# Performance work log

Hardware: AMD Instinct MI355X
Metric: run time of the kernel (lower is better)

Reference implementation:

```python
import jax, jax.numpy as jnp
import numpy as np

# Model constants (from init_kwargs)
N_EMBD = 1024
N_HEAD = 16
HEAD_DIM = N_EMBD // N_HEAD  # 64
SEQ = 32       # new tokens (ds.input_ids)
PAST = 32768   # cached tokens (ds.past)
NEG = -10000.0 # module uses -1e4, not -inf


def setup_inputs() -> dict:
    key = jax.random.key(0)
    ks = jax.random.split(key, 5)
    return {
        "x": jax.random.normal(ks[0], (SEQ, N_EMBD), jnp.float32),
        "layer_past": jax.random.normal(ks[1], (2, N_HEAD, PAST, HEAD_DIM), jnp.float32) * 0.02,
        "w_attn": jax.random.normal(ks[2], (N_EMBD, 3 * N_EMBD), jnp.float32) * 0.02,
        "b_attn": jnp.zeros((3 * N_EMBD,), jnp.float32),
        "w_proj": jax.random.normal(ks[3], (N_EMBD, N_EMBD), jnp.float32) * 0.02,
        "b_proj": jnp.zeros((N_EMBD,), jnp.float32),
        "seq_len": SEQ,
        "past_len": PAST,
    }


def reference(x, layer_past, w_attn, b_attn, w_proj, b_proj, seq_len, past_len):
    # c_attn (Conv1D): x @ W + b, W is [nx, nf]
    qkv = x @ w_attn + b_attn                      # [S, 3E]
    qkv = qkv.reshape(seq_len, 3, N_EMBD)
    # split_heads: [S, E] -> [S, H, D] -> [H, S, D]
    def split(t):
        return t.reshape(seq_len, N_HEAD, HEAD_DIM).transpose(1, 0, 2)
    q, k, v = split(qkv[:, 0]), split(qkv[:, 1]), split(qkv[:, 2])
    # KV-cache concat along time
    key_full = jnp.concatenate([layer_past[0], k], axis=1)   # [H, P+S, D]
    val_full = jnp.concatenate([layer_past[1], v], axis=1)   # [H, P+S, D]
    present = jnp.stack([key_full, val_full])                # [2, H, P+S, D]
    tot_len = past_len + seq_len
    # scores
    w = jnp.einsum("hsd,htd->hst", q, key_full) / float(np.sqrt(HEAD_DIM))
    # causal mask: query at abs position past+i sees keys 0..past+i
    mask = jnp.arange(tot_len)[None, :] <= (past_len + jnp.arange(seq_len))[:, None]
    w = jnp.where(mask[None, :, :], w, NEG)
    w = jax.nn.softmax(w, axis=-1)
    a = jnp.einsum("hst,htd->hsd", w, val_full)              # [H, S, D]
    # merge_heads: [H, S, D] -> [S, H, D] -> [S, E]
    a = a.transpose(1, 0, 2).reshape(seq_len, N_EMBD)
    out = a @ w_proj + b_proj                                # [S, E]
    return (out, present)
```

## Files before the change

### kernel.cpp

```cpp
#include <hip/hip_runtime.h>

#define HEADS 16
#define SEQL 32
#define HD 64
#define PASTN 32768
#define TOTN 32800
#define NE 1024
#define CHUNK 1024
#define NPC 32
#define NCHUNK 33
#define KT 64
#define LDP 68
#define NEGV -10000.0f

__global__ __launch_bounds__(256) void qkv_kernel(
    const float* __restrict__ x, const float* __restrict__ w,
    const float* __restrict__ b, float* __restrict__ qws,
    float* __restrict__ present)
{
    int idx = blockIdx.x * 256 + threadIdx.x;
    int s = idx / 3072;
    int col = idx - s * 3072;
    const float4* x4 = (const float4*)(x + s * NE);
    float a0 = 0.f, a1 = 0.f, a2 = 0.f, a3 = 0.f;
#pragma unroll 8
    for (int k4 = 0; k4 < NE / 4; ++k4) {
        float4 xv = x4[k4];
        const float* wp = w + (k4 * 4) * 3072 + col;
        a0 = fmaf(xv.x, wp[0],        a0);
        a1 = fmaf(xv.y, wp[3072],     a1);
        a2 = fmaf(xv.z, wp[2 * 3072], a2);
        a3 = fmaf(xv.w, wp[3 * 3072], a3);
    }
    float acc = b[col] + ((a0 + a1) + (a2 + a3));
    int g = col >> 10;
    int e = col & 1023;
    int h = e >> 6, d = e & 63;
    if (g == 0)
        qws[(h * SEQL + s) * HD + d] = acc;
    else
        present[(((g - 1) * HEADS + h) * TOTN + PASTN + s) * HD + d] = acc;
}

__global__ __launch_bounds__(256) void attn_partial(
    const float* __restrict__ past, const float* __restrict__ qws,
    float* __restrict__ present, float* __restrict__ opart,
    float* __restrict__ mws, float* __restrict__ lws)
{
    int h = blockIdx.x / NCHUNK;
    int c = blockIdx.x - h * NCHUNK;
    __shared__ __align__(16) float Qs[SEQL][LDP];
    __shared__ __align__(16) float Ks[KT][LDP];
    __shared__ __align__(16) float Vs[KT][LDP];
    __shared__ __align__(16) float Ss[SEQL][LDP];
    __shared__ float mrow[SEQL], lrow[SEQL], arow[SEQL];
    int tid = threadIdx.x;

    for (int i = tid; i < SEQL * 16; i += 256) {
        int q = i >> 4, s4 = i & 15;
        *(float4*)&Qs[q][s4 * 4] = *(const float4*)&qws[(h * SEQL + q) * HD + s4 * 4];
    }
    if (tid < SEQL) { mrow[tid] = -3e38f; lrow[tid] = 0.f; }

    float4 acc4[4];
#pragma unroll
    for (int j = 0; j < 4; ++j) acc4[j] = make_float4(0.f, 0.f, 0.f, 0.f);

    int qg = tid >> 4;
    int lg = tid & 15;
    int nkeys = (c < NPC) ? CHUNK : KT;
    int kstart = c * CHUNK;
    __syncthreads();

    for (int t0 = 0; t0 < nkeys; t0 += KT) {
        if (c < NPC) {
#pragma unroll
            for (int rep = 0; rep < 4; ++rep) {
                int i = tid + rep * 256;
                int row = i >> 4, s4 = i & 15;
                int grow = kstart + t0 + row;
                float4 kk = *(const float4*)&past[(h * PASTN + grow) * HD + s4 * 4];
                float4 vv = *(const float4*)&past[((HEADS + h) * PASTN + grow) * HD + s4 * 4];
                *(float4*)&present[(h * TOTN + grow) * HD + s4 * 4] = kk;
                *(float4*)&present[((HEADS + h) * TOTN + grow) * HD + s4 * 4] = vv;
                *(float4*)&Ks[row][s4 * 4] = kk;
                *(float4*)&Vs[row][s4 * 4] = vv;
            }
        } else {
            float* vz = &Vs[SEQL][0];
            for (int i = tid; i < (KT - SEQL) * LDP; i += 256) vz[i] = 0.f;
#pragma unroll
            for (int rep = 0; rep < 2; ++rep) {
                int i = tid + rep * 256;
                int row = i >> 4, s4 = i & 15;
                int grow = PASTN + row;
                float4 kk = *(const float4*)&present[(h * TOTN + grow) * HD + s4 * 4];
                float4 vv = *(const float4*)&present[((HEADS + h) * TOTN + grow) * HD + s4 * 4];
                *(float4*)&Ks[row][s4 * 4] = kk;
                *(float4*)&Vs[row][s4 * 4] = vv;
            }
        }
        __syncthreads();

        if (tid < 128) {
            float s[4][4];
#pragma unroll
            for (int j = 0; j < 4; ++j)
#pragma unroll
                for (int u = 0; u < 4; ++u) s[j][u] = 0.f;
#pragma unroll
            for (int d4 = 0; d4 < 16; ++d4) {
                float4 qv[4], kv[4];
#pragma unroll
                for (int j = 0; j < 4; ++j)
                    qv[j] = *(const float4*)&Qs[qg * 4 + j][d4 * 4];
#pragma unroll
                for (int u = 0; u < 4; ++u)
                    kv[u] = *(const float4*)&Ks[lg + u * 16][d4 * 4];
#pragma unroll
                for (int j = 0; j < 4; ++j)
#pragma unroll
                    for (int u = 0; u < 4; ++u) {
                        s[j][u] = fmaf(qv[j].x, kv[u].x, s[j][u]);
                        s[j][u] = fmaf(qv[j].y, kv[u].y, s[j][u]);
                        s[j][u] = fmaf(qv[j].z, kv[u].z, s[j][u]);
                        s[j][u] = fmaf(qv[j].w, kv[u].w, s[j][u]);
                    }
            }
#pragma unroll
            for (int j = 0; j < 4; ++j) {
                int q = qg * 4 + j;
#pragma unroll
                for (int u = 0; u < 4; ++u) {
                    float sv = s[j][u] * 0.125f;
                    if (c == NPC && (lg + u * 16) > q) sv = NEGV;
                    Ss[q][lg + u * 16] = sv;
                }
            }
        }
        __syncthreads();

        {
            int q = tid >> 3, sub = tid & 7;
            float v[8];
#pragma unroll
            for (int i = 0; i < 8; ++i) v[i] = Ss[q][sub + 8 * i];
            float mt = fmaxf(fmaxf(fmaxf(v[0], v[1]), fmaxf(v[2], v[3])),
                             fmaxf(fmaxf(v[4], v[5]), fmaxf(v[6], v[7])));
            mt = fmaxf(mt, __shfl_xor(mt, 1));
            mt = fmaxf(mt, __shfl_xor(mt, 2));
            mt = fmaxf(mt, __shfl_xor(mt, 4));
            float mold = mrow[q];
            float mnew = fmaxf(mold, mt);
            float ls = 0.f;
#pragma unroll
            for (int i = 0; i < 8; ++i) {
                float p = __expf(v[i] - mnew);
                Ss[q][sub + 8 * i] = p;
                ls += p;
            }
            ls += __shfl_xor(ls, 1);
            ls += __shfl_xor(ls, 2);
            ls += __shfl_xor(ls, 4);
            if (sub == 0) {
                float alpha = __expf(mold - mnew);
                lrow[q] = lrow[q] * alpha + ls;
                mrow[q] = mnew;
                arow[q] = alpha;
            }
        }
        __syncthreads();

        if (tid < 128) {
#pragma unroll
            for (int j = 0; j < 4; ++j) {
                float aj = arow[qg * 4 + j];
                acc4[j].x *= aj; acc4[j].y *= aj; acc4[j].z *= aj; acc4[j].w *= aj;
            }
#pragma unroll
            for (int t4 = 0; t4 < 16; ++t4) {
                float4 vv[4];
#pragma unroll
                for (int u = 0; u < 4; ++u)
                    vv[u] = *(const float4*)&Vs[t4 * 4 + u][lg * 4];
#pragma unroll
                for (int j = 0; j < 4; ++j) {
                    float4 p = *(const float4*)&Ss[qg * 4 + j][t4 * 4];
                    acc4[j].x = fmaf(p.x, vv[0].x, acc4[j].x);
                    acc4[j].x = fmaf(p.y, vv[1].x, acc4[j].x);
                    acc4[j].x = fmaf(p.z, vv[2].x, acc4[j].x);
                    acc4[j].x = fmaf(p.w, vv[3].x, acc4[j].x);
                    acc4[j].y = fmaf(p.x, vv[0].y, acc4[j].y);
                    acc4[j].y = fmaf(p.y, vv[1].y, acc4[j].y);
                    acc4[j].y = fmaf(p.z, vv[2].y, acc4[j].y);
                    acc4[j].y = fmaf(p.w, vv[3].y, acc4[j].y);
                    acc4[j].z = fmaf(p.x, vv[0].z, acc4[j].z);
                    acc4[j].z = fmaf(p.y, vv[1].z, acc4[j].z);
                    acc4[j].z = fmaf(p.z, vv[2].z, acc4[j].z);
                    acc4[j].z = fmaf(p.w, vv[3].z, acc4[j].z);
                    acc4[j].w = fmaf(p.x, vv[0].w, acc4[j].w);
                    acc4[j].w = fmaf(p.y, vv[1].w, acc4[j].w);
                    acc4[j].w = fmaf(p.z, vv[2].w, acc4[j].w);
                    acc4[j].w = fmaf(p.w, vv[3].w, acc4[j].w);
                }
            }
        }
        __syncthreads();
    }

    if (tid < SEQL) {
        mws[(h * NCHUNK + c) * SEQL + tid] = mrow[tid];
        lws[(h * NCHUNK + c) * SEQL + tid] = lrow[tid];
    }
    if (tid < 128) {
#pragma unroll
        for (int j = 0; j < 4; ++j) {
            int q = qg * 4 + j;
            *(float4*)&opart[((h * NCHUNK + c) * SEQL + q) * HD + lg * 4] = acc4[j];
        }
    }
}

__global__ __launch_bounds__(64) void attn_reduce(
    const float* __restrict__ opart, const float* __restrict__ mws,
    const float* __restrict__ lws, float* __restrict__ aws)
{
    int h = blockIdx.x >> 5;
    int q = blockIdx.x & 31;
    int d = threadIdx.x;
    float M = -3e38f;
    for (int c = 0; c < NCHUNK; ++c)
        M = fmaxf(M, mws[(h * NCHUNK + c) * SEQL + q]);
    float L = 0.f, o = 0.f;
    for (int c = 0; c < NCHUNK; ++c) {
        float wgt = __expf(mws[(h * NCHUNK + c) * SEQL + q] - M);
        L = fmaf(lws[(h * NCHUNK + c) * SEQL + q], wgt, L);
        o = fmaf(opart[((h * NCHUNK + c) * SEQL + q) * HD + d], wgt, o);
    }
    aws[q * NE + h * HD + d] = o / L;
}

__global__ __launch_bounds__(256) void proj_kernel(
    const float* __restrict__ aws, const float* __restrict__ w,
    const float* __restrict__ b, float* __restrict__ out)
{
    int idx = blockIdx.x * 256 + threadIdx.x;
    int s = idx >> 10, e = idx & 1023;
    const float4* a4 = (const float4*)(aws + s * NE);
    float a0 = 0.f, a1 = 0.f, a2 = 0.f, a3 = 0.f;
#pragma unroll 8
    for (int k4 = 0; k4 < NE / 4; ++k4) {
        float4 xv = a4[k4];
        const float* wp = w + (k4 * 4) * NE + e;
        a0 = fmaf(xv.x, wp[0],      a0);
        a1 = fmaf(xv.y, wp[NE],     a1);
        a2 = fmaf(xv.z, wp[2 * NE], a2);
        a3 = fmaf(xv.w, wp[3 * NE], a3);
    }
    out[idx] = b[e] + ((a0 + a1) + (a2 + a3));
}

extern "C" void kernel_launch(void* const* d_in, const int* in_sizes, int n_in,
                              void* d_out, int out_size, void* d_ws, size_t ws_size,
                              hipStream_t stream) {
    const float* x      = (const float*)d_in[0];
    const float* past   = (const float*)d_in[1];
    const float* w_attn = (const float*)d_in[2];
    const float* b_attn = (const float*)d_in[3];
    const float* w_proj = (const float*)d_in[4];
    const float* b_proj = (const float*)d_in[5];

    float* out     = (float*)d_out;
    float* present = out + SEQL * NE;

    float* wsf   = (float*)d_ws;
    float* qws   = wsf;
    float* aws   = wsf + 32768;
    float* mws   = wsf + 65536;
    float* lws   = mws + 16896;
    float* opart = lws + 16896;

    qkv_kernel<<<(SEQL * 3072) / 256, 256, 0, stream>>>(x, w_attn, b_attn, qws, present);
    attn_partial<<<HEADS * NCHUNK, 256, 0, stream>>>(past, qws, present, opart, mws, lws);
    attn_reduce<<<HEADS * SEQL, 64, 0, stream>>>(opart, mws, lws, aws);
    proj_kernel<<<(SEQL * NE) / 256, 256, 0, stream>>>(aws, w_proj, b_proj, out);
}
```

Baseline: 579.7 us.

## Prefetch KV tiles into registers and fuse online softmax into compute threads

Restructures the attention partial kernel so the next 64-key K/V tile is loaded into registers while the current tile is computed, then written to present and shared memory. The online-softmax max/sum reduction moves from a separate block-wide phase into the score threads, using 16-lane shuffles with per-thread running max and sum registers. This removes two barriers per tile and the shared mrow/lrow arrays. It adds launch_bounds(256,2) as an occupancy hint. It raises register pressure from the prefetch buffers and uses an inline lgkmcnt wait to order the shared-memory writes before they are read back.

Result: slower. 622.4 us (+7.4%).

```diff
diff --git a/kernel.cpp b/kernel.cpp
--- a/kernel.cpp
+++ b/kernel.cpp
@@ -42,7 +42,105 @@
         present[(((g - 1) * HEADS + h) * TOTN + PASTN + s) * HD + d] = acc;
 }
 
-__global__ __launch_bounds__(256) void attn_partial(
+template<int NT, bool MASK>
+__device__ __forceinline__ void compute_tile(
+    float (&Qs)[SEQL][LDP], float (&Ks)[KT][LDP],
+    float (&Vs)[KT][LDP], float (&Ss)[SEQL][LDP],
+    int qg, int lg, float4 (&acc4)[4], float (&mreg)[4], float (&lreg)[4])
+{
+    constexpr int NU = NT / 16;
+    float s[4][NU];
+#pragma unroll
+    for (int j = 0; j < 4; ++j)
+#pragma unroll
+        for (int u = 0; u < NU; ++u) s[j][u] = 0.f;
+#pragma unroll
+    for (int d4 = 0; d4 < 16; ++d4) {
+        float4 qv[4], kv[NU];
+#pragma unroll
+        for (int j = 0; j < 4; ++j)
+            qv[j] = *(const float4*)&Qs[qg * 4 + j][d4 * 4];
+#pragma unroll
+        for (int u = 0; u < NU; ++u)
+            kv[u] = *(const float4*)&Ks[lg + u * 16][d4 * 4];
+#pragma unroll
+        for (int j = 0; j < 4; ++j)
+#pragma unroll
+            for (int u = 0; u < NU; ++u) {
+                s[j][u] = fmaf(qv[j].x, kv[u].x, s[j][u]);
+                s[j][u] = fmaf(qv[j].y, kv[u].y, s[j][u]);
+                s[j][u] = fmaf(qv[j].z, kv[u].z, s[j][u]);
+                s[j][u] = fmaf(qv[j].w, kv[u].w, s[j][u]);
+            }
+    }
+    float alpha[4];
+#pragma unroll
+    for (int j = 0; j < 4; ++j) {
+        int q = qg * 4 + j;
+        float mt = -3e38f;
+#pragma unroll
+        for (int u = 0; u < NU; ++u) {
+            float sv = s[j][u] * 0.125f;
+            if (MASK && (lg + 16 * u) > q) sv = NEGV;
+            s[j][u] = sv;
+            mt = fmaxf(mt, sv);
+        }
+        mt = fmaxf(mt, __shfl_xor(mt, 1));
+        mt = fmaxf(mt, __shfl_xor(mt, 2));
+        mt = fmaxf(mt, __shfl_xor(mt, 4));
+        mt = fmaxf(mt, __shfl_xor(mt, 8));
+        float mnew = fmaxf(mreg[j], mt);
+        alpha[j] = __expf(mreg[j] - mnew);
+        mreg[j] = mnew;
+        float ps = 0.f;
+#pragma unroll
+        for (int u = 0; u < NU; ++u) {
+            float p = __expf(s[j][u] - mnew);
+            Ss[q][lg + 16 * u] = p;
+            ps += p;
+        }
+        ps += __shfl_xor(ps, 1);
+        ps += __shfl_xor(ps, 2);
+        ps += __shfl_xor(ps, 4);
+        ps += __shfl_xor(ps, 8);
+        lreg[j] = lreg[j] * alpha[j] + ps;
+    }
+    asm volatile("s_waitcnt lgkmcnt(0)" ::: "memory");
+#pragma unroll
+    for (int j = 0; j < 4; ++j) {
+        acc4[j].x *= alpha[j]; acc4[j].y *= alpha[j];
+        acc4[j].z *= alpha[j]; acc4[j].w *= alpha[j];
+    }
+#pragma unroll
+    for (int t4 = 0; t4 < NT / 4; ++t4) {
+        float4 vvv[4];
+#pragma unroll
+        for (int u = 0; u < 4; ++u)
+            vvv[u] = *(const float4*)&Vs[t4 * 4 + u][lg * 4];
+#pragma unroll
+        for (int j = 0; j < 4; ++j) {
+            float4 p = *(const float4*)&Ss[qg * 4 + j][t4 * 4];
+            acc4[j].x = fmaf(p.x, vvv[0].x, acc4[j].x);
+            acc4[j].x = fmaf(p.y, vvv[1].x, acc4[j].x);
+            acc4[j].x = fmaf(p.z, vvv[2].x, acc4[j].x);
+            acc4[j].x = fmaf(p.w, vvv[3].x, acc4[j].x);
+            acc4[j].y = fmaf(p.x, vvv[0].y, acc4[j].y);
+            acc4[j].y = fmaf(p.y, vvv[1].y, acc4[j].y);
+            acc4[j].y = fmaf(p.z, vvv[2].y, acc4[j].y);
+            acc4[j].y = fmaf(p.w, vvv[3].y, acc4[j].y);
+            acc4[j].z = fmaf(p.x, vvv[0].z, acc4[j].z);
+            acc4[j].z = fmaf(p.y, vvv[1].z, acc4[j].z);
+            acc4[j].z = fmaf(p.z, vvv[2].z, acc4[j].z);
+            acc4[j].z = fmaf(p.w, vvv[3].z, acc4[j].z);
+            acc4[j].w = fmaf(p.x, vvv[0].w, acc4[j].w);
+            acc4[j].w = fmaf(p.y, vvv[1].w, acc4[j].w);
+            acc4[j].w = fmaf(p.z, vvv[2].w, acc4[j].w);
+            acc4[j].w = fmaf(p.w, vvv[3].w, acc4[j].w);
+        }
+    }
+}
+
+__global__ __launch_bounds__(256, 2) void attn_partial(
     const float* __restrict__ past, const float* __restrict__ qws,
     float* __restrict__ present, float* __restrict__ opart,
     float* __restrict__ mws, float* __restrict__ lws)
@@ -53,171 +151,90 @@
     __shared__ __align__(16) float Ks[KT][LDP];
     __shared__ __align__(16) float Vs[KT][LDP];
     __shared__ __align__(16) float Ss[SEQL][LDP];
-    __shared__ float mrow[SEQL], lrow[SEQL], arow[SEQL];
     int tid = threadIdx.x;
 
     for (int i = tid; i < SEQL * 16; i += 256) {
-        int q = i >> 4, s4 = i & 15;
-        *(float4*)&Qs[q][s4 * 4] = *(const float4*)&qws[(h * SEQL + q) * HD + s4 * 4];
-    }
-    if (tid < SEQL) { mrow[tid] = -3e38f; lrow[tid] = 0.f; }
+        int q = i >> 4, s4i = i & 15;
+        *(float4*)&Qs[q][s4i * 4] = *(const float4*)&qws[(h * SEQL + q) * HD + s4i * 4];
+    }
 
     float4 acc4[4];
-#pragma unroll
-    for (int j = 0; j < 4; ++j) acc4[j] = make_float4(0.f, 0.f, 0.f, 0.f);
-
+    float mreg[4], lreg[4];
+#pragma unroll
+    for (int j = 0; j < 4; ++j) {
+        acc4[j] = make_float4(0.f, 0.f, 0.f, 0.f);
+        mreg[j] = -3e38f;
+        lreg[j] = 0.f;
+    }
     int qg = tid >> 4;
     int lg = tid & 15;
-    int nkeys = (c < NPC) ? CHUNK : KT;
-    int kstart = c * CHUNK;
-    __syncthreads();
-
-    for (int t0 = 0; t0 < nkeys; t0 += KT) {
-        if (c < NPC) {
-#pragma unroll
-            for (int rep = 0; rep < 4; ++rep) {
-                int i = tid + rep * 256;
-                int row = i >> 4, s4 = i & 15;
-                int grow = kstart + t0 + row;
-                float4 kk = *(const float4*)&past[(h * PASTN + grow) * HD + s4 * 4];
-                float4 vv = *(const float4*)&past[((HEADS + h) * PASTN + grow) * HD + s4 * 4];
-                *(float4*)&present[(h * TOTN + grow) * HD + s4 * 4] = kk;
-                *(float4*)&present[((HEADS + h) * TOTN + grow) * HD + s4 * 4] = vv;
-                *(float4*)&Ks[row][s4 * 4] = kk;
-                *(float4*)&Vs[row][s4 * 4] = vv;
-            }
-        } else {
-            float* vz = &Vs[SEQL][0];
-            for (int i = tid; i < (KT - SEQL) * LDP; i += 256) vz[i] = 0.f;
-#pragma unroll
-            for (int rep = 0; rep < 2; ++rep) {
-                int i = tid + rep * 256;
-                int row = i >> 4, s4 = i & 15;
-                int grow = PASTN + row;
-                float4 kk = *(const float4*)&present[(h * TOTN + grow) * HD + s4 * 4];
-                float4 vv = *(const float4*)&present[((HEADS + h) * TOTN + grow) * HD + s4 * 4];
-                *(float4*)&Ks[row][s4 * 4] = kk;
-                *(float4*)&Vs[row][s4 * 4] = vv;
-            }
-        }
+
+    if (c < NPC) {
+        int kstart = c * CHUNK;
+        int row = tid >> 4;
+        int s4 = tid & 15;
+        float4 kk[4], vv[4];
+
+        auto loadT = [&](int t0) {
+#pragma unroll
+            for (int r = 0; r < 4; ++r) {
+                int grow = kstart + t0 + row + r * 16;
+                kk[r] = *(const float4*)&past[(h * PASTN + grow) * HD + s4 * 4];
+                vv[r] = *(const float4*)&past[((HEADS + h) * PASTN + grow) * HD + s4 * 4];
+            }
+        };
+        auto writeT = [&](int t0) {
+#pragma unroll
+            for (int r = 0; r < 4; ++r) {
+                int grow = kstart + t0 + row + r * 16;
+                *(float4*)&present[(h * TOTN + grow) * HD + s4 * 4] = kk[r];
+                *(float4*)&present[((HEADS + h) * TOTN + grow) * HD + s4 * 4] = vv[r];
+                *(float4*)&Ks[row + r * 16][s4 * 4] = kk[r];
+                *(float4*)&Vs[row + r * 16][s4 * 4] = vv[r];
+            }
+        };
+
+        loadT(0);
         __syncthreads();
-
-        if (tid < 128) {
-            float s[4][4];
-#pragma unroll
-            for (int j = 0; j < 4; ++j)
-#pragma unroll
-                for (int u = 0; u < 4; ++u) s[j][u] = 0.f;
-#pragma unroll
-            for (int d4 = 0; d4 < 16; ++d4) {
-                float4 qv[4], kv[4];
-#pragma unroll
-                for (int j = 0; j < 4; ++j)
-                    qv[j] = *(const float4*)&Qs[qg * 4 + j][d4 * 4];
-#pragma unroll
-                for (int u = 0; u < 4; ++u)
-                    kv[u] = *(const float4*)&Ks[lg + u * 16][d4 * 4];
-#pragma unroll
-                for (int j = 0; j < 4; ++j)
-#pragma unroll
-                    for (int u = 0; u < 4; ++u) {
-                        s[j][u] = fmaf(qv[j].x, kv[u].x, s[j][u]);
-                        s[j][u] = fmaf(qv[j].y, kv[u].y, s[j][u]);
-                        s[j][u] = fmaf(qv[j].z, kv[u].z, s[j][u]);
-                        s[j][u] = fmaf(qv[j].w, kv[u].w, s[j][u]);
-                    }
-            }
+        writeT(0);
+        __syncthreads();
+        for (int t0 = 0; t0 < CHUNK; t0 += KT) {
+            bool pf = (t0 + KT) < CHUNK;
+            if (pf) loadT(t0 + KT);
+            if (tid < 128)
+                compute_tile<KT, false>(Qs, Ks, Vs, Ss, qg, lg, acc4, mreg, lreg);
+            if (pf) {
+                __syncthreads();
+                writeT(t0 + KT);
+                __syncthreads();
+            }
+        }
+    } else {
+        int row = tid >> 4;
+        int s4 = tid & 15;
+#pragma unroll
+        for (int r = 0; r < 2; ++r) {
+            int rw = row + r * 16;
+            int grow = PASTN + rw;
+            *(float4*)&Ks[rw][s4 * 4] = *(const float4*)&present[(h * TOTN + grow) * HD + s4 * 4];
+            *(float4*)&Vs[rw][s4 * 4] = *(const float4*)&present[((HEADS + h) * TOTN + grow) * HD + s4 * 4];
+        }
+        __syncthreads();
+        if (tid < 128)
+            compute_tile<SEQL, true>(Qs, Ks, Vs, Ss, qg, lg, acc4, mreg, lreg);
+    }
+
+    if (tid < 128) {
+        if (lg == 0) {
 #pragma unroll
             for (int j = 0; j < 4; ++j) {
-                int q = qg * 4 + j;
-#pragma unroll
-                for (int u = 0; u < 4; ++u) {
-                    float sv = s[j][u] * 0.125f;
-                    if (c == NPC && (lg + u * 16) > q) sv = NEGV;
-                    Ss[q][lg + u * 16] = sv;
-                }
-            }
-        }
-        __syncthreads();
-
-        {
-            int q = tid >> 3, sub = tid & 7;
-            float v[8];
-#pragma unroll
-            for (int i = 0; i < 8; ++i) v[i] = Ss[q][sub + 8 * i];
-            float mt = fmaxf(fmaxf(fmaxf(v[0], v[1]), fmaxf(v[2], v[3])),
-                             fmaxf(fmaxf(v[4], v[5]), fmaxf(v[6], v[7])));
-            mt = fmaxf(mt, __shfl_xor(mt, 1));
-            mt = fmaxf(mt, __shfl_xor(mt, 2));
-            mt = fmaxf(mt, __shfl_xor(mt, 4));
-            float mold = mrow[q];
-            float mnew = fmaxf(mold, mt);
-            float ls = 0.f;
-#pragma unroll
-            for (int i = 0; i < 8; ++i) {
-                float p = __expf(v[i] - mnew);
-                Ss[q][sub + 8 * i] = p;
-                ls += p;
-            }
-            ls += __shfl_xor(ls, 1);
-            ls += __shfl_xor(ls, 2);
-            ls += __shfl_xor(ls, 4);
-            if (sub == 0) {
-                float alpha = __expf(mold - mnew);
-                lrow[q] = lrow[q] * alpha + ls;
-                mrow[q] = mnew;
-                arow[q] = alpha;
-            }
-        }
-        __syncthreads();
-
-        if (tid < 128) {
-#pragma unroll
-            for (int j = 0; j < 4; ++j) {
-                float aj = arow[qg * 4 + j];
-                acc4[j].x *= aj; acc4[j].y *= aj; acc4[j].z *= aj; acc4[j].w *= aj;
-            }
-#pragma unroll
-            for (int t4 = 0; t4 < 16; ++t4) {
-                float4 vv[4];
-#pragma unroll
-                for (int u = 0; u < 4; ++u)
-                    vv[u] = *(const float4*)&Vs[t4 * 4 + u][lg * 4];
-#pragma unroll
-                for (int j = 0; j < 4; ++j) {
-                    float4 p = *(const float4*)&Ss[qg * 4 + j][t4 * 4];
-                    acc4[j].x = fmaf(p.x, vv[0].x, acc4[j].x);
-                    acc4[j].x = fmaf(p.y, vv[1].x, acc4[j].x);
-                    acc4[j].x = fmaf(p.z, vv[2].x, acc4[j].x);
-                    acc4[j].x = fmaf(p.w, vv[3].x, acc4[j].x);
-                    acc4[j].y = fmaf(p.x, vv[0].y, acc4[j].y);
-                    acc4[j].y = fmaf(p.y, vv[1].y, acc4[j].y);
-                    acc4[j].y = fmaf(p.z, vv[2].y, acc4[j].y);
-                    acc4[j].y = fmaf(p.w, vv[3].y, acc4[j].y);
-                    acc4[j].z = fmaf(p.x, vv[0].z, acc4[j].z);
-                    acc4[j].z = fmaf(p.y, vv[1].z, acc4[j].z);
-                    acc4[j].z = fmaf(p.z, vv[2].z, acc4[j].z);
-                    acc4[j].z = fmaf(p.w, vv[3].z, acc4[j].z);
-                    acc4[j].w = fmaf(p.x, vv[0].w, acc4[j].w);
-                    acc4[j].w = fmaf(p.y, vv[1].w, acc4[j].w);
-                    acc4[j].w = fmaf(p.z, vv[2].w, acc4[j].w);
-                    acc4[j].w = fmaf(p.w, vv[3].w, acc4[j].w);
-                }
-            }
-        }
-        __syncthreads();
-    }
-
-    if (tid < SEQL) {
-        mws[(h * NCHUNK + c) * SEQL + tid] = mrow[tid];
-        lws[(h * NCHUNK + c) * SEQL + tid] = lrow[tid];
-    }
-    if (tid < 128) {
-#pragma unroll
-        for (int j = 0; j < 4; ++j) {
-            int q = qg * 4 + j;
-            *(float4*)&opart[((h * NCHUNK + c) * SEQL + q) * HD + lg * 4] = acc4[j];
-        }
+                mws[(h * NCHUNK + c) * SEQL + qg * 4 + j] = mreg[j];
+                lws[(h * NCHUNK + c) * SEQL + qg * 4 + j] = lreg[j];
+            }
+        }
+#pragma unroll
+        for (int j = 0; j < 4; ++j)
+            *(float4*)&opart[((h * NCHUNK + c) * SEQL + qg * 4 + j) * HD + lg * 4] = acc4[j];
     }
 }
 
```
